# Optimization experiments

Hardware: AMD Instinct MI355X
Metric: run time of the kernel (lower is better)

The kernel has to match this reference:

```python
import jax, jax.numpy as jnp
import numpy as np
from jax import lax


def setup_inputs() -> dict:
    key = jax.random.key(0)
    k1, k2, k3, k4 = jax.random.split(key, 4)
    D = 128
    B = 16
    image = jax.random.normal(k1, (1, D, D, D), jnp.float32)          # [1, D, H, W]
    x = jax.random.normal(k2, (B, 1, D, D, D), jnp.float32)           # [B, 1, D, H, W]
    # Conv3d(1, 27, kernel_size=3) parameters
    W = jax.random.normal(k3, (27, 1, 3, 3, 3), jnp.float32) * (1.0 / np.sqrt(27.0))
    b = jax.random.normal(k4, (27,), jnp.float32) * 0.01
    return {"image": image, "x": x, "W": W, "b": b}


def reference(image, x, W, b):
    D, H, Wd = image.shape[1], image.shape[2], image.shape[3]
    # K = Conv3d(image): per-voxel 27 filter taps. Unbatched CDHW -> add batch dim.
    K = lax.conv_general_dilated(
        image[None], W, window_strides=(1, 1, 1), padding='SAME',
        dimension_numbers=('NCDHW', 'OIDHW', 'NCDHW'))[0]             # [27, D, H, W]
    K = K + b[:, None, None, None]
    # permute (1,2,3,0) + unflatten(3,(3,3,3)) -> [D, H, W, 3, 3, 3]
    K = jnp.moveaxis(K, 0, -1).reshape(D, H, Wd, 3, 3, 3)
    # Apply dynamic per-voxel 3x3x3 filter: sum of 27 shifted slices
    xp = jnp.pad(x, ((0, 0), (0, 0), (1, 1), (1, 1), (1, 1)))         # [B,1,D+2,H+2,W+2]
    y = jnp.zeros_like(x)
    for di in range(3):
        for dj in range(3):
            for dk in range(3):
                tap = K[..., di, dj, dk][None, None]                  # [1,1,D,H,W]
                y = y + tap * xp[:, :, di:di + D, dj:dj + H, dk:dk + Wd]
    return y
```

## Files before the change

kernel.cpp:

```cpp
#include <hip/hip_runtime.h>

typedef __fp16 f16x2 __attribute__((ext_vector_type(2)));

#define Dm 128
#define Bn 16
#define TZ 4
#define TYt 8
#define TXv 16
#define HY 10
#define WPR 12
#define TILE_W 768
#define NT 256
#define NPAIR 3
#define VOX (Dm * Dm * Dm)
#define BCH 4
#define NCH (Bn / BCH)

__device__ __forceinline__ int iclamp(int v, int lo, int hi) {
  return v < lo ? lo : (v > hi ? hi : v);
}
__device__ __forceinline__ f16x2 pkrtz(float lo, float hi) {
  return __builtin_amdgcn_cvt_pkrtz(lo, hi);
}
__device__ __forceinline__ float pkbits(float lo, float hi) {
  return __builtin_bit_cast(float, __builtin_amdgcn_cvt_pkrtz(lo, hi));
}
__device__ __forceinline__ f16x2 asf16x2(float w) {
  return __builtin_bit_cast(f16x2, w);
}
__device__ __forceinline__ f16x2 midpair(f16x2 h23, f16x2 h01) {
  unsigned r = __builtin_amdgcn_perm(__builtin_bit_cast(unsigned, h23),
                                     __builtin_bit_cast(unsigned, h01),
                                     0x05040302u);
  return __builtin_bit_cast(f16x2, r);
}

extern "C" __global__ void packW(const float* __restrict__ Wf,
                                 const float* __restrict__ bfp,
                                 float* __restrict__ wpk) {
  int i = threadIdx.x;
  if (i < 729) {
    int o = i / 27, t = i - o * 27;
    float v = Wf[i];
    wpk[t * 27 + o] = pkbits(v, v);
  } else if (i < 756) {
    float b = bfp[i - 729];
    wpk[i] = pkbits(b, b);
  }
}

extern "C" __global__ void __launch_bounds__(NT, 4)
fused3d(const float* __restrict__ img, const float* __restrict__ x,
        const float* __restrict__ wpk, float* __restrict__ out)
{
  __shared__ float sImgP[TILE_W];
  __shared__ float sXP[2][BCH][TILE_W];

  const int tid = threadIdx.x;
  const int tx = tid & 7;
  const int ty = (tid >> 3) & 7;
  const int tz = tid >> 6;

  const int bid = blockIdx.x;
  const int s  = (bid & 7) * 512 + (bid >> 3);
  const int bx = s & 7, by = (s >> 3) & 15, bz = s >> 7;
  const int w0 = bx * TXv, h0 = by * TYt, d0 = bz * TZ;

  int off0[NPAIR], off1[NPAIR];
  float oki0[NPAIR], oki1[NPAIR];
#pragma unroll
  for (int k = 0; k < NPAIR; ++k) {
    int p  = k * NT + tid;
    int r  = p / WPR;
    int c  = 2 * (p - r * WPR);
    int zz = r / HY;
    int yy = r - zz * HY;
    int gd = d0 + zz - 1, gh = h0 + yy - 1;
    int g0 = w0 + c - 1,  g1 = w0 + c;
    int base = (iclamp(gd, 0, Dm - 1) * Dm + iclamp(gh, 0, Dm - 1)) * Dm;
    off0[k] = base + iclamp(g0, 0, Dm - 1);
    off1[k] = base + iclamp(g1, 0, Dm - 1);
    bool rk = ((unsigned)gd < Dm) & ((unsigned)gh < Dm);
    oki0[k] = (rk & ((unsigned)g0 < Dm)) ? 1.f : 0.f;
    oki1[k] = (rk & ((unsigned)g1 < Dm)) ? 1.f : 0.f;
  }

  {
    float ri0[NPAIR], ri1[NPAIR];
#pragma unroll
    for (int k = 0; k < NPAIR; ++k) {
      ri0[k] = img[off0[k]] * oki0[k];
      ri1[k] = img[off1[k]] * oki1[k];
    }
    float rx0[BCH][NPAIR], rx1[BCH][NPAIR];
#pragma unroll
    for (int j = 0; j < BCH; ++j)
#pragma unroll
      for (int k = 0; k < NPAIR; ++k) {
        rx0[j][k] = x[(size_t)j * VOX + off0[k]];
        rx1[j][k] = x[(size_t)j * VOX + off1[k]];
      }
#pragma unroll
    for (int k = 0; k < NPAIR; ++k)
      sImgP[k * NT + tid] = pkbits(ri0[k], ri1[k]);
#pragma unroll
    for (int j = 0; j < BCH; ++j)
#pragma unroll
      for (int k = 0; k < NPAIR; ++k)
        sXP[0][j][k * NT + tid] = pkbits(rx0[j][k], rx1[j][k]);
  }
  __syncthreads();

  float nx0[BCH][NPAIR], nx1[BCH][NPAIR];
#pragma unroll
  for (int j = 0; j < BCH; ++j)
#pragma unroll
    for (int k = 0; k < NPAIR; ++k) {
      nx0[j][k] = x[(size_t)(BCH + j) * VOX + off0[k]];
      nx1[j][k] = x[(size_t)(BCH + j) * VOX + off1[k]];
    }

  const int tbase = (tz * HY + ty) * WPR + tx;
  f16x2 K2[27];
#pragma unroll
  for (int o = 0; o < 27; ++o) K2[o] = asf16x2(wpk[729 + o]);
#pragma unroll
  for (int rr = 0; rr < 9; ++rr) {
    const int wofs = tbase + ((rr / 3) * HY + (rr % 3)) * WPR;
    float u0 = sImgP[wofs], u1 = sImgP[wofs + 1];
    f16x2 h01 = asf16x2(u0), h23 = asf16x2(u1), h12 = midpair(h23, h01);
    const float* wA = wpk + (rr * 3 + 0) * 27;
    const float* wB = wpk + (rr * 3 + 1) * 27;
    const float* wC = wpk + (rr * 3 + 2) * 27;
#pragma unroll
    for (int o = 0; o < 27; ++o) {
      K2[o] = __builtin_elementwise_fma(asf16x2(wA[o]), h01, K2[o]);
      K2[o] = __builtin_elementwise_fma(asf16x2(wB[o]), h12, K2[o]);
      K2[o] = __builtin_elementwise_fma(asf16x2(wC[o]), h23, K2[o]);
    }
  }

  const int od = d0 + tz, oh = h0 + ty, ow = w0 + 2 * tx;
#pragma unroll
  for (int o = 0; o < 27; ++o) {
    const int di = o / 9, dj = (o / 3) % 3, dk = o % 3;
    const bool mm = ((unsigned)(od + di - 1) < Dm) & ((unsigned)(oh + dj - 1) < Dm);
    const float m0 = (mm & ((unsigned)(ow + dk - 1) < Dm)) ? 1.f : 0.f;
    const float m1 = (mm & ((unsigned)(ow + dk)     < Dm)) ? 1.f : 0.f;
    K2[o] *= pkrtz(m0, m1);
  }

  const size_t obase = (((size_t)od) * Dm + oh) * Dm + ow;

  for (int ch = 0; ch < NCH; ++ch) {
    const int cur = ch & 1;

#pragma unroll
    for (int j = 0; j < BCH; ++j) {
      const float* sx = sXP[cur][j];
      f16x2 aA = {(__fp16)0.f, (__fp16)0.f};
      f16x2 aB = {(__fp16)0.f, (__fp16)0.f};
#pragma unroll
      for (int rr = 0; rr < 9; ++rr) {
        const int wofs = tbase + ((rr / 3) * HY + (rr % 3)) * WPR;
        float u0 = sx[wofs], u1 = sx[wofs + 1];
        f16x2 h01 = asf16x2(u0), h23 = asf16x2(u1), h12 = midpair(h23, h01);
        if (rr & 1) {
          aB = __builtin_elementwise_fma(K2[rr * 3 + 0], h01, aB);
          aB = __builtin_elementwise_fma(K2[rr * 3 + 1], h12, aB);
          aB = __builtin_elementwise_fma(K2[rr * 3 + 2], h23, aB);
        } else {
          aA = __builtin_elementwise_fma(K2[rr * 3 + 0], h01, aA);
          aA = __builtin_elementwise_fma(K2[rr * 3 + 1], h12, aA);
          aA = __builtin_elementwise_fma(K2[rr * 3 + 2], h23, aA);
        }
      }
      f16x2 acc = aA + aB;
      float2 st; st.x = (float)acc.x; st.y = (float)acc.y;
      *(float2*)&out[(size_t)(ch * BCH + j) * VOX + obase] = st;
    }

    if (ch + 1 < NCH) {
#pragma unroll
      for (int j = 0; j < BCH; ++j)
#pragma unroll
        for (int k = 0; k < NPAIR; ++k)
          sXP[cur ^ 1][j][k * NT + tid] = pkbits(nx0[j][k], nx1[j][k]);
    }

    __syncthreads();

    if (ch + 2 < NCH) {
      const float* xc = x + (size_t)(ch + 2) * BCH * VOX;
#pragma unroll
      for (int j = 0; j < BCH; ++j)
#pragma unroll
        for (int k = 0; k < NPAIR; ++k) {
          nx0[j][k] = xc[(size_t)j * VOX + off0[k]];
          nx1[j][k] = xc[(size_t)j * VOX + off1[k]];
        }
    }
  }
}

extern "C" void kernel_launch(void* const* d_in, const int* in_sizes, int n_in,
                              void* d_out, int out_size, void* d_ws, size_t ws_size,
                              hipStream_t stream) {
  const float* img = (const float*)d_in[0];
  const float* x   = (const float*)d_in[1];
  const float* Wf  = (const float*)d_in[2];
  const float* bf  = (const float*)d_in[3];
  float* out = (float*)d_out;
  float* wpk = (float*)d_ws;
  hipLaunchKernelGGL(packW, dim3(1), dim3(768), 0, stream, Wf, bf, wpk);
  hipLaunchKernelGGL(fused3d, dim3(4096), dim3(256), 0, stream, img, x, wpk, out);
}
```

Baseline: 128.8 us.

## Use per-wave LDS slabs with aligned float2 loads and barrier-free batch loop

Each wavefront now owns one output depth slice and loads its own 3-slice halo into a private LDS slab. Because no LDS data is shared across waves, the __syncthreads barriers go away. Global loads become aligned float2 pairs, and the batch loop processes one batch at a time, prefetching the next batch in registers. The smaller LDS footprint allows launch bounds of 8 blocks per CU, at the cost of redundant halo reads across waves and less memory-level parallelism per wave.

```diff
diff --git a/kernel.cpp b/kernel.cpp
--- a/kernel.cpp
+++ b/kernel.cpp
@@ -4,17 +4,10 @@
 
 #define Dm 128
 #define Bn 16
-#define TZ 4
-#define TYt 8
-#define TXv 16
-#define HY 10
-#define WPR 12
-#define TILE_W 768
+#define VOX (Dm * Dm * Dm)
 #define NT 256
-#define NPAIR 3
-#define VOX (Dm * Dm * Dm)
-#define BCH 4
-#define NCH (Bn / BCH)
+#define WR 10
+#define SLAB 320
 
 __device__ __forceinline__ int iclamp(int v, int lo, int hi) {
   return v < lo ? lo : (v > hi ? hi : v);
@@ -28,9 +21,9 @@
 __device__ __forceinline__ f16x2 asf16x2(float w) {
   return __builtin_bit_cast(f16x2, w);
 }
-__device__ __forceinline__ f16x2 midpair(f16x2 h23, f16x2 h01) {
-  unsigned r = __builtin_amdgcn_perm(__builtin_bit_cast(unsigned, h23),
-                                     __builtin_bit_cast(unsigned, h01),
+__device__ __forceinline__ f16x2 midpair(f16x2 P, f16x2 Q) {
+  unsigned r = __builtin_amdgcn_perm(__builtin_bit_cast(unsigned, P),
+                                     __builtin_bit_cast(unsigned, Q),
                                      0x05040302u);
   return __builtin_bit_cast(f16x2, r);
 }
@@ -49,86 +42,70 @@
   }
 }
 
-extern "C" __global__ void __launch_bounds__(NT, 4)
+extern "C" __global__ void __launch_bounds__(NT, 8)
 fused3d(const float* __restrict__ img, const float* __restrict__ x,
         const float* __restrict__ wpk, float* __restrict__ out)
 {
-  __shared__ float sImgP[TILE_W];
-  __shared__ float sXP[2][BCH][TILE_W];
+  __shared__ float sImg[4][SLAB];
+  __shared__ float sXw[4][SLAB];
 
-  const int tid = threadIdx.x;
-  const int tx = tid & 7;
-  const int ty = (tid >> 3) & 7;
-  const int tz = tid >> 6;
+  const int tid  = threadIdx.x;
+  const int lane = tid & 63;
+  const int wv   = tid >> 6;
+  const int tx   = lane & 7;
+  const int ty   = lane >> 3;
 
   const int bid = blockIdx.x;
   const int s  = (bid & 7) * 512 + (bid >> 3);
   const int bx = s & 7, by = (s >> 3) & 15, bz = s >> 7;
-  const int w0 = bx * TXv, h0 = by * TYt, d0 = bz * TZ;
+  const int w0 = bx * 16, h0 = by * 8, d0 = bz * 4;
 
-  int off0[NPAIR], off1[NPAIR];
-  float oki0[NPAIR], oki1[NPAIR];
+  int off[5];
+  float mk0[5], mk1[5];
 #pragma unroll
-  for (int k = 0; k < NPAIR; ++k) {
-    int p  = k * NT + tid;
-    int r  = p / WPR;
-    int c  = 2 * (p - r * WPR);
-    int zz = r / HY;
-    int yy = r - zz * HY;
-    int gd = d0 + zz - 1, gh = h0 + yy - 1;
-    int g0 = w0 + c - 1,  g1 = w0 + c;
-    int base = (iclamp(gd, 0, Dm - 1) * Dm + iclamp(gh, 0, Dm - 1)) * Dm;
-    off0[k] = base + iclamp(g0, 0, Dm - 1);
-    off1[k] = base + iclamp(g1, 0, Dm - 1);
-    bool rk = ((unsigned)gd < Dm) & ((unsigned)gh < Dm);
-    oki0[k] = (rk & ((unsigned)g0 < Dm)) ? 1.f : 0.f;
-    oki1[k] = (rk & ((unsigned)g1 < Dm)) ? 1.f : 0.f;
+  for (int k = 0; k < 5; ++k) {
+    int i  = 64 * k + lane;
+    int r  = i / WR;
+    int c  = i - r * WR;
+    int zz = r / 10;
+    int yy = r - zz * 10;
+    int gdo = d0 + wv + zz - 1;
+    int gho = h0 + yy - 1;
+    int gwo = w0 - 2 + 2 * c;
+    int gd = iclamp(gdo, 0, Dm - 1);
+    int gh = iclamp(gho, 0, Dm - 1);
+    int gw = iclamp(gwo, 0, Dm - 2);
+    off[k] = (gd * Dm + gh) * Dm + gw;
+    bool rk = ((unsigned)gdo < Dm) & ((unsigned)gho < Dm);
+    mk0[k] = (rk & ((unsigned)gwo < Dm))       ? 1.f : 0.f;
+    mk1[k] = (rk & ((unsigned)(gwo + 1) < Dm)) ? 1.f : 0.f;
   }
 
-  {
-    float ri0[NPAIR], ri1[NPAIR];
+  float* simg = sImg[wv];
+  float* sxw  = sXw[wv];
+
 #pragma unroll
-    for (int k = 0; k < NPAIR; ++k) {
-      ri0[k] = img[off0[k]] * oki0[k];
-      ri1[k] = img[off1[k]] * oki1[k];
-    }
-    float rx0[BCH][NPAIR], rx1[BCH][NPAIR];
+  for (int k = 0; k < 5; ++k) {
+    float2 v = *(const float2*)(img + off[k]);
+    simg[64 * k + lane] = pkbits(v.x * mk0[k], v.y * mk1[k]);
+  }
+  float2 nx[5];
 #pragma unroll
-    for (int j = 0; j < BCH; ++j)
-#pragma unroll
-      for (int k = 0; k < NPAIR; ++k) {
-        rx0[j][k] = x[(size_t)j * VOX + off0[k]];
-        rx1[j][k] = x[(size_t)j * VOX + off1[k]];
-      }
-#pragma unroll
-    for (int k = 0; k < NPAIR; ++k)
-      sImgP[k * NT + tid] = pkbits(ri0[k], ri1[k]);
-#pragma unroll
-    for (int j = 0; j < BCH; ++j)
-#pragma unroll
-      for (int k = 0; k < NPAIR; ++k)
-        sXP[0][j][k * NT + tid] = pkbits(rx0[j][k], rx1[j][k]);
-  }
-  __syncthreads();
+  for (int k = 0; k < 5; ++k)
+    nx[k] = *(const float2*)(x + off[k]);
 
-  float nx0[BCH][NPAIR], nx1[BCH][NPAIR];
-#pragma unroll
-  for (int j = 0; j < BCH; ++j)
-#pragma unroll
-    for (int k = 0; k < NPAIR; ++k) {
-      nx0[j][k] = x[(size_t)(BCH + j) * VOX + off0[k]];
-      nx1[j][k] = x[(size_t)(BCH + j) * VOX + off1[k]];
-    }
-
-  const int tbase = (tz * HY + ty) * WPR + tx;
   f16x2 K2[27];
 #pragma unroll
   for (int o = 0; o < 27; ++o) K2[o] = asf16x2(wpk[729 + o]);
 #pragma unroll
   for (int rr = 0; rr < 9; ++rr) {
-    const int wofs = tbase + ((rr / 3) * HY + (rr % 3)) * WPR;
-    float u0 = sImgP[wofs], u1 = sImgP[wofs + 1];
-    f16x2 h01 = asf16x2(u0), h23 = asf16x2(u1), h12 = midpair(h23, h01);
+    const int idx = ((rr / 3) * 10 + ty + (rr % 3)) * WR + tx;
+    f16x2 a2 = asf16x2(simg[idx]);
+    f16x2 b2 = asf16x2(simg[idx + 1]);
+    f16x2 c2 = asf16x2(simg[idx + 2]);
+    f16x2 h01 = midpair(b2, a2);
+    f16x2 h12 = b2;
+    f16x2 h23 = midpair(c2, b2);
     const float* wA = wpk + (rr * 3 + 0) * 27;
     const float* wB = wpk + (rr * 3 + 1) * 27;
     const float* wC = wpk + (rr * 3 + 2) * 27;
@@ -140,7 +117,7 @@
     }
   }
 
-  const int od = d0 + tz, oh = h0 + ty, ow = w0 + 2 * tx;
+  const int od = d0 + wv, oh = h0 + ty, ow = w0 + 2 * tx;
 #pragma unroll
   for (int o = 0; o < 27; ++o) {
     const int di = o / 9, dj = (o / 3) % 3, dk = o % 3;
@@ -152,54 +129,41 @@
 
   const size_t obase = (((size_t)od) * Dm + oh) * Dm + ow;
 
-  for (int ch = 0; ch < NCH; ++ch) {
-    const int cur = ch & 1;
+#pragma unroll 1
+  for (int b = 0; b < Bn; ++b) {
+#pragma unroll
+    for (int k = 0; k < 5; ++k)
+      sxw[64 * k + lane] = pkbits(nx[k].x, nx[k].y);
 
+    const float* xb = x + (size_t)(b + 1 < Bn ? b + 1 : Bn - 1) * VOX;
 #pragma unroll
-    for (int j = 0; j < BCH; ++j) {
-      const float* sx = sXP[cur][j];
-      f16x2 aA = {(__fp16)0.f, (__fp16)0.f};
-      f16x2 aB = {(__fp16)0.f, (__fp16)0.f};
+    for (int k = 0; k < 5; ++k)
+      nx[k] = *(const float2*)(xb + off[k]);
+
+    f16x2 aA = {(__fp16)0.f, (__fp16)0.f};
+    f16x2 aB = {(__fp16)0.f, (__fp16)0.f};
 #pragma unroll
-      for (int rr = 0; rr < 9; ++rr) {
-        const int wofs = tbase + ((rr / 3) * HY + (rr % 3)) * WPR;
-        float u0 = sx[wofs], u1 = sx[wofs + 1];
-        f16x2 h01 = asf16x2(u0), h23 = asf16x2(u1), h12 = midpair(h23, h01);
-        if (rr & 1) {
-          aB = __builtin_elementwise_fma(K2[rr * 3 + 0], h01, aB);
-          aB = __builtin_elementwise_fma(K2[rr * 3 + 1], h12, aB);
-          aB = __builtin_elementwise_fma(K2[rr * 3 + 2], h23, aB);
-        } else {
-          aA = __builtin_elementwise_fma(K2[rr * 3 + 0], h01, aA);
-          aA = __builtin_elementwise_fma(K2[rr * 3 + 1], h12, aA);
-          aA = __builtin_elementwise_fma(K2[rr * 3 + 2], h23, aA);
-        }
+    for (int rr = 0; rr < 9; ++rr) {
+      const int idx = ((rr / 3) * 10 + ty + (rr % 3)) * WR + tx;
+      f16x2 a2 = asf16x2(sxw[idx]);
+      f16x2 b2 = asf16x2(sxw[idx + 1]);
+      f16x2 c2 = asf16x2(sxw[idx + 2]);
+      f16x2 h01 = midpair(b2, a2);
+      f16x2 h12 = b2;
+      f16x2 h23 = midpair(c2, b2);
+      if (rr & 1) {
+        aB = __builtin_elementwise_fma(K2[rr * 3 + 0], h01, aB);
+        aB = __builtin_elementwise_fma(K2[rr * 3 + 1], h12, aB);
+        aB = __builtin_elementwise_fma(K2[rr * 3 + 2], h23, aB);
+      } else {
+        aA = __builtin_elementwise_fma(K2[rr * 3 + 0], h01, aA);
+        aA = __builtin_elementwise_fma(K2[rr * 3 + 1], h12, aA);
+        aA = __builtin_elementwise_fma(K2[rr * 3 + 2], h23, aA);
       }
-      f16x2 acc = aA + aB;
-      float2 st; st.x = (float)acc.x; st.y = (float)acc.y;
-      *(float2*)&out[(size_t)(ch * BCH + j) * VOX + obase] = st;
     }
-
-    if (ch + 1 < NCH) {
-#pragma unroll
-      for (int j = 0; j < BCH; ++j)
-#pragma unroll
-        for (int k = 0; k < NPAIR; ++k)
-          sXP[cur ^ 1][j][k * NT + tid] = pkbits(nx0[j][k], nx1[j][k]);
-    }
-
-    __syncthreads();
-
-    if (ch + 2 < NCH) {
-      const float* xc = x + (size_t)(ch + 2) * BCH * VOX;
-#pragma unroll
-      for (int j = 0; j < BCH; ++j)
-#pragma unroll
-        for (int k = 0; k < NPAIR; ++k) {
-          nx0[j][k] = xc[(size_t)j * VOX + off0[k]];
-          nx1[j][k] = xc[(size_t)j * VOX + off1[k]];
-        }
-    }
+    f16x2 acc = aA + aB;
+    float2 st; st.x = (float)acc.x; st.y = (float)acc.y;
+    *(float2*)&out[(size_t)b * VOX + obase] = st;
   }
 }
 
@@ -213,5 +177,5 @@
   float* out = (float*)d_out;
   float* wpk = (float*)d_ws;
   hipLaunchKernelGGL(packW, dim3(1), dim3(768), 0, stream, Wf, bf, wpk);
-  hipLaunchKernelGGL(fused3d, dim3(4096), dim3(256), 0, stream, img, x, wpk, out);
+  hipLaunchKernelGGL(fused3d, dim3(4096), dim3(NT), 0, stream, img, x, wpk, out);
 }
```

Result: slower. 166.3 us (+29.0%).
